# Kernel optimization log

Measured on AMD Instinct MI355X. Metric: run time of the kernel, lower is better.

The kernel has to match this reference:

```python
import jax, jax.numpy as jnp
import numpy as np

N = 80000        # nodes
E = 1280000      # edges
NG = 8           # graphs (segment ids)
F_IN = 3
NC = 20
BN_EPS = 1e-3    # keras BatchNormalization default epsilon


def setup_inputs() -> dict:
    key = jax.random.key(0)
    ks = jax.random.split(key, 16)
    inp = {}
    inp['x'] = jax.random.normal(ks[0], (N, F_IN), dtype=jnp.float32)
    inp['edge_w'] = jax.random.uniform(ks[1], (E,), dtype=jnp.float32)
    inp['src'] = jax.random.randint(ks[2], (E,), 0, N, dtype=jnp.int32)
    inp['dst'] = jax.random.randint(ks[3], (E,), 0, N, dtype=jnp.int32)
    inp['ids'] = jnp.sort(jax.random.randint(ks[4], (N,), 0, NG, dtype=jnp.int32))
    def w(k, fi, fo):
        return jax.random.normal(k, (fi, fo), dtype=jnp.float32) * (1.0 / np.sqrt(fi))
    inp['W1'] = w(ks[5], F_IN, 32); inp['b1'] = jnp.zeros((32,), jnp.float32)
    inp['W2'] = w(ks[6], 32, 32);   inp['b2'] = jnp.zeros((32,), jnp.float32)
    inp['g1'] = jnp.ones((32,), jnp.float32); inp['be1'] = jnp.zeros((32,), jnp.float32)
    inp['m1'] = jax.random.normal(ks[7], (32,), dtype=jnp.float32) * 0.1
    inp['v1'] = jax.random.uniform(ks[8], (32,), dtype=jnp.float32) + 0.5
    inp['W3'] = w(ks[9], 32, 64);   inp['b3'] = jnp.zeros((64,), jnp.float32)
    inp['W4'] = w(ks[10], 64, 64);  inp['b4'] = jnp.zeros((64,), jnp.float32)
    inp['g2'] = jnp.ones((64,), jnp.float32); inp['be2'] = jnp.zeros((64,), jnp.float32)
    inp['m2'] = jax.random.normal(ks[11], (64,), dtype=jnp.float32) * 0.1
    inp['v2'] = jax.random.uniform(ks[12], (64,), dtype=jnp.float32) + 0.5
    inp['W5'] = w(ks[13], 64, NC);  inp['b5'] = jnp.zeros((NC,), jnp.float32)
    return inp


def _gcn(x, W, b, src, dst, ew):
    # Spektral GCNConv: A_norm @ (X W) + b, with A given as edge list (src->dst).
    h = x @ W                                      # [N, Fo] dense transform first (cheaper)
    msg = h[src] * ew[:, None]                     # gather + scale  [E, Fo]
    agg = jax.ops.segment_sum(msg, dst, num_segments=N)  # scatter-add [N, Fo]
    return agg + b


def _bn(x, g, be, m, v):
    # inference-mode BatchNormalization
    return (x - m) * (g * jax.lax.rsqrt(v + BN_EPS)) + be


def _pool(x, ids):
    # per-graph global max pooling, broadcast back to nodes
    mx = jax.ops.segment_max(x, ids, num_segments=NG)   # [NG, F]
    return mx[ids]                                       # [N, F]


def reference(x, edge_w, src, dst, ids,
              W1, b1, W2, b2, g1, be1, m1, v1,
              W3, b3, W4, b4, g2, be2, m2, v2,
              W5, b5):
    h = jax.nn.relu(_gcn(x, W1, b1, src, dst, edge_w))
    h = jax.nn.relu(_gcn(h, W2, b2, src, dst, edge_w))
    h = _bn(h, g1, be1, m1, v1)
    h = _pool(h, ids)
    h = jax.nn.relu(_gcn(h, W3, b3, src, dst, edge_w))
    h = jax.nn.relu(_gcn(h, W4, b4, src, dst, edge_w))
    h = _bn(h, g2, be2, m2, v2)
    h = _pool(h, ids)
    # dropout is identity in inference
    out = jax.nn.softmax(_gcn(h, W5, b5, src, dst, edge_w), axis=-1)
    return out
```

## Files before the change

kernel.cpp:

```cpp
#include <hip/hip_runtime.h>

#define NN 80000
#define NE 1280000
#define NGR 8
#define BN_EPS 1e-3f
#define NBF 625
#define GB 1280
#define CHK 1000

typedef unsigned short ushort;
typedef __attribute__((ext_vector_type(8))) short bf16x8;
typedef __attribute__((ext_vector_type(4))) float f32x4;

__device__ __forceinline__ unsigned enc_f(float f) {
    unsigned b = __float_as_uint(f);
    return (f >= 0.f) ? (b | 0x80000000u) : ~b;
}
__device__ __forceinline__ float dec_f(unsigned u) {
    return (u & 0x80000000u) ? __uint_as_float(u & 0x7FFFFFFFu) : __uint_as_float(~u);
}
__device__ __forceinline__ ushort f2bf(float f) {
    unsigned u = __float_as_uint(f);
    unsigned r = u + 0x7FFFu + ((u >> 16) & 1u);
    return (ushort)(r >> 16);
}
__device__ __forceinline__ void fma8(float* acc, const ushort* p, float w) {
    uint4 q = *(const uint4*)p;
    acc[0] += w * __uint_as_float((q.x & 0xFFFFu) << 16);
    acc[1] += w * __uint_as_float(q.x & 0xFFFF0000u);
    acc[2] += w * __uint_as_float((q.y & 0xFFFFu) << 16);
    acc[3] += w * __uint_as_float(q.y & 0xFFFF0000u);
    acc[4] += w * __uint_as_float((q.z & 0xFFFFu) << 16);
    acc[5] += w * __uint_as_float(q.z & 0xFFFF0000u);
    acc[6] += w * __uint_as_float((q.w & 0xFFFFu) << 16);
    acc[7] += w * __uint_as_float(q.w & 0xFFFF0000u);
}

__global__ __launch_bounds__(256) void k_bhist(const int* __restrict__ dst,
                                               int* __restrict__ hcnt) {
    __shared__ int lh[NBF];
    for (int i = threadIdx.x; i < NBF; i += 256) lh[i] = 0;
    __syncthreads();
    int e0 = blockIdx.x * CHK;
    for (int e = e0 + threadIdx.x; e < e0 + CHK; e += 256)
        atomicAdd(&lh[dst[e] >> 7], 1);
    __syncthreads();
    int* row = hcnt + (size_t)blockIdx.x * NBF;
    for (int i = threadIdx.x; i < NBF; i += 256) row[i] = lh[i];
}

__global__ __launch_bounds__(256) void k_bbase1(int* __restrict__ hcnt,
                                                int* __restrict__ tot) {
    __shared__ int sm[256];
    int bin = blockIdx.x, t = threadIdx.x;
    int v[5];
    int s = 0;
    #pragma unroll
    for (int j = 0; j < 5; ++j) {
        v[j] = hcnt[(size_t)(t * 5 + j) * NBF + bin];
        s += v[j];
    }
    sm[t] = s;
    __syncthreads();
    #pragma unroll
    for (int off = 1; off < 256; off <<= 1) {
        int u = (t >= off) ? sm[t - off] : 0;
        __syncthreads();
        sm[t] += u;
        __syncthreads();
    }
    int run = sm[t] - s;
    if (t == 255) tot[bin] = sm[255];
    #pragma unroll
    for (int j = 0; j < 5; ++j) {
        hcnt[(size_t)(t * 5 + j) * NBF + bin] = run;
        run += v[j];
    }
}

__global__ __launch_bounds__(1024) void k_bbase2w(const int* __restrict__ tot,
                                                  int* __restrict__ bo,
                                                  const float* __restrict__ W2,
                                                  const float* __restrict__ W4,
                                                  ushort* __restrict__ W2t,
                                                  ushort* __restrict__ W4t) {
    __shared__ int sm[1024];
    int t = threadIdx.x;
    int v = (t < NBF) ? tot[t] : 0;
    sm[t] = v;
    __syncthreads();
    #pragma unroll
    for (int off = 1; off < 1024; off <<= 1) {
        int u = (t >= off) ? sm[t - off] : 0;
        __syncthreads();
        sm[t] += u;
        __syncthreads();
    }
    if (t < NBF) bo[t] = sm[t] - v;
    if (t == 0) bo[NBF] = NE;
    {
        int f = t >> 5, k = t & 31;
        W2t[t] = f2bf(W2[k * 32 + f]);
    }
    #pragma unroll
    for (int j = 0; j < 4; ++j) {
        int i = t + j * 1024;
        int f = i >> 6, k = i & 63;
        W4t[i] = f2bf(W4[k * 64 + f]);
    }
}

__global__ __launch_bounds__(256) void k_bfill(const int* __restrict__ src,
                                               const int* __restrict__ dst,
                                               const float* __restrict__ ew,
                                               const int* __restrict__ ids,
                                               const int* __restrict__ hcnt,
                                               const int* __restrict__ bo,
                                               int2* __restrict__ cB) {
    __shared__ int lcur[NBF];
    const int* row = hcnt + (size_t)blockIdx.x * NBF;
    for (int i = threadIdx.x; i < NBF; i += 256) lcur[i] = row[i] + bo[i];
    __syncthreads();
    int e0 = blockIdx.x * CHK;
    for (int e = e0 + threadIdx.x; e < e0 + CHK; e += 256) {
        int d = dst[e];
        int s = src[e];
        int pos = atomicAdd(&lcur[d >> 7], 1);
        cB[pos] = make_int2(s | (ids[s] << 17) | ((d & 127) << 20),
                            __float_as_int(ew[e]));
    }
}

__global__ __launch_bounds__(512) void k_insort(const int* __restrict__ bo,
                                                const int2* __restrict__ cB,
                                                const float* __restrict__ x,
                                                int* __restrict__ rp,
                                                int2* __restrict__ cE,
                                                float* __restrict__ S,
                                                float* __restrict__ AX) {
    __shared__ int lc[128];
    __shared__ int loff[128];
    __shared__ int sm[512];
    int bin = blockIdx.x, t = threadIdx.x;
    int s0 = bo[bin], s1 = bo[bin + 1];
    if (t < 128) lc[t] = 0;
    __syncthreads();
    for (int i = s0 + t; i < s1; i += 512)
        atomicAdd(&lc[(cB[i].x >> 20) & 127], 1);
    __syncthreads();
    int v = (t < 128) ? lc[t] : 0;
    sm[t] = v;
    __syncthreads();
    #pragma unroll
    for (int off = 1; off < 128; off <<= 1) {
        int u = (t >= off && t < 128) ? sm[t - off] : 0;
        __syncthreads();
        if (t < 128) sm[t] += u;
        __syncthreads();
    }
    if (t < 128) {
        loff[t] = sm[t] - v;
        rp[bin * 128 + t] = s0 + loff[t];
        lc[t] = 0;
    }
    if (bin == NBF - 1 && t == 0) rp[NN] = NE;
    __syncthreads();
    for (int i = s0 + t; i < s1; i += 512) {
        int2 a = cB[i];
        int dlow = (a.x >> 20) & 127;
        int pos = s0 + loff[dlow] + atomicAdd(&lc[dlow], 1);
        cE[pos] = make_int2((a.x & 0x1FFFF) | (((a.x >> 17) & 7) << 24), a.y);
    }
    __syncthreads();
    int n = t >> 2, q = t & 3;
    int ne0 = s0 + loff[n];
    int ne1 = ne0 + lc[n];
    float sv[8] = {0, 0, 0, 0, 0, 0, 0, 0};
    float ax0 = 0.f, ax1 = 0.f, ax2 = 0.f;
    for (int i = ne0 + q; i < ne1; i += 4) {
        int2 a = cE[i];
        float w = __int_as_float(a.y);
        int s = a.x & 0xFFFFFF;
        int gg = a.x >> 24;
        #pragma unroll
        for (int g = 0; g < 8; ++g) sv[g] += (gg == g) ? w : 0.f;
        const float* xp = x + s * 3;
        ax0 += w * xp[0]; ax1 += w * xp[1]; ax2 += w * xp[2];
    }
    #pragma unroll
    for (int g = 0; g < 8; ++g) {
        sv[g] += __shfl_xor(sv[g], 1);
        sv[g] += __shfl_xor(sv[g], 2);
    }
    ax0 += __shfl_xor(ax0, 1); ax0 += __shfl_xor(ax0, 2);
    ax1 += __shfl_xor(ax1, 1); ax1 += __shfl_xor(ax1, 2);
    ax2 += __shfl_xor(ax2, 1); ax2 += __shfl_xor(ax2, 2);
    if (q == 0) {
        int node = bin * 128 + n;
        float4* Sp = (float4*)(S + (size_t)node * 8);
        Sp[0] = make_float4(sv[0], sv[1], sv[2], sv[3]);
        Sp[1] = make_float4(sv[4], sv[5], sv[6], sv[7]);
        *(float4*)(AX + (size_t)node * 4) = make_float4(ax0, ax1, ax2, 0.f);
    }
}

__global__ __launch_bounds__(256) void k_gpl2(const float* __restrict__ AX,
                                              const float* __restrict__ W1,
                                              const float* __restrict__ b1,
                                              const ushort* __restrict__ W2t,
                                              const int* __restrict__ rp,
                                              const int2* __restrict__ cE,
                                              const int* __restrict__ ids,
                                              const float* __restrict__ b2,
                                              const float* __restrict__ g1,
                                              const float* __restrict__ be1,
                                              const float* __restrict__ m1,
                                              const float* __restrict__ v1,
                                              unsigned* __restrict__ mxe) {
    __shared__ unsigned lmx[NGR * 32];
    __shared__ ushort aggS[64 * 40];
    __shared__ int gids[64];
    int t = threadIdx.x;
    int nb = blockIdx.x * 64;
    lmx[t] = 0u;
    if (t < 64) gids[t] = ids[nb + t];
    int c = t & 3;
    float w1r0[8], w1r1[8], w1r2[8], b1c[8];
    #pragma unroll
    for (int j = 0; j < 8; ++j) {
        int f = c * 8 + j;
        w1r0[j] = W1[f]; w1r1[j] = W1[32 + f]; w1r2[j] = W1[64 + f];
        b1c[j] = b1[f];
    }
    int nl = t >> 2;
    int n = nb + nl;
    int e0 = rp[n], e1 = rp[n + 1];
    float acc[8] = {0, 0, 0, 0, 0, 0, 0, 0};
    for (int i = e0; i < e1; ++i) {
        int2 a = cE[i];
        float w = __int_as_float(a.y);
        float axv = AX[(size_t)(a.x & 0xFFFFFF) * 4 + c];
        float a0 = __shfl(axv, 0, 4);
        float a1 = __shfl(axv, 1, 4);
        float a2 = __shfl(axv, 2, 4);
        #pragma unroll
        for (int j = 0; j < 8; ++j) {
            float pre = b1c[j] + a0 * w1r0[j] + a1 * w1r1[j] + a2 * w1r2[j];
            acc[j] += w * fmaxf(pre, 0.f);
        }
    }
    #pragma unroll
    for (int j = 0; j < 8; ++j) aggS[nl * 40 + c * 8 + j] = f2bf(acc[j]);
    __syncthreads();
    int lane = t & 63, wave = t >> 6;
    int quad = lane >> 4, col = lane & 15;
    bf16x8 afr = *(const bf16x8*)(aggS + (wave * 16 + col) * 40 + quad * 8);
    #pragma unroll
    for (int nt = 0; nt < 2; ++nt) {
        bf16x8 bfr = *(const bf16x8*)(W2t + (nt * 16 + col) * 32 + quad * 8);
        f32x4 d = {0.f, 0.f, 0.f, 0.f};
        d = __builtin_amdgcn_mfma_f32_16x16x32_bf16(afr, bfr, d, 0, 0, 0);
        int f = nt * 16 + col;
        float scale = g1[f] * rsqrtf(v1[f] + BN_EPS);
        float bb = b2[f], mm = m1[f], bee = be1[f];
        #pragma unroll
        for (int r = 0; r < 4; ++r) {
            int node_l = wave * 16 + quad * 4 + r;
            float h = fmaxf(d[r] + bb, 0.f);
            float val = (h - mm) * scale + bee;
            atomicMax(&lmx[gids[node_l] * 32 + f], enc_f(val));
        }
    }
    __syncthreads();
    {
        unsigned u = lmx[t];
        if (u) atomicMax(&mxe[t], u);
    }
}

__global__ __launch_bounds__(256) void k_l34m(const float* __restrict__ S,
                                              const unsigned* __restrict__ mxe,
                                              const float* __restrict__ W3,
                                              const float* __restrict__ b3,
                                              const ushort* __restrict__ W4t,
                                              ushort* __restrict__ T) {
    __shared__ float smxs[256];
    __shared__ float HW3s[512];
    __shared__ ushort h3s[64 * 72];
    int t = threadIdx.x;
    int nb = blockIdx.x * 64;
    smxs[t] = mxe[t] ? dec_f(mxe[t]) : 0.f;
    __syncthreads();
    {
        #pragma unroll
        for (int j = 0; j < 2; ++j) {
            int i = t + j * 256;
            int g = i >> 6, f = i & 63;
            float acc = 0.f;
            #pragma unroll
            for (int k = 0; k < 32; ++k) acc += smxs[g * 32 + k] * W3[k * 64 + f];
            HW3s[i] = acc;
        }
    }
    __syncthreads();
    {
        int f = t & 63, rr = t >> 6;
        float hwc[8];
        #pragma unroll
        for (int g = 0; g < 8; ++g) hwc[g] = HW3s[g * 64 + f];
        float bb = b3[f];
        #pragma unroll
        for (int i = 0; i < 16; ++i) {
            int n = rr + i * 4;
            const float4* sp = (const float4*)(S + (size_t)(nb + n) * 8);
            float4 s0 = sp[0], s1 = sp[1];
            float acc = bb + s0.x * hwc[0] + s0.y * hwc[1] + s0.z * hwc[2] +
                        s0.w * hwc[3] + s1.x * hwc[4] + s1.y * hwc[5] +
                        s1.z * hwc[6] + s1.w * hwc[7];
            h3s[n * 72 + f] = f2bf(fmaxf(acc, 0.f));
        }
    }
    __syncthreads();
    int lane = t & 63, wave = t >> 6;
    int quad = lane >> 4, col = lane & 15;
    int mtile = wave;
    bf16x8 a0 = *(const bf16x8*)(h3s + (mtile * 16 + col) * 72 + quad * 8);
    bf16x8 a1 = *(const bf16x8*)(h3s + (mtile * 16 + col) * 72 + 32 + quad * 8);
    #pragma unroll
    for (int ntile = 0; ntile < 4; ++ntile) {
        bf16x8 b0 = *(const bf16x8*)(W4t + (ntile * 16 + col) * 64 + quad * 8);
        bf16x8 b1v = *(const bf16x8*)(W4t + (ntile * 16 + col) * 64 + 32 + quad * 8);
        f32x4 acc = {0.f, 0.f, 0.f, 0.f};
        acc = __builtin_amdgcn_mfma_f32_16x16x32_bf16(a0, b0, acc, 0, 0, 0);
        acc = __builtin_amdgcn_mfma_f32_16x16x32_bf16(a1, b1v, acc, 0, 0, 0);
        #pragma unroll
        for (int r = 0; r < 4; ++r) {
            int node = nb + mtile * 16 + quad * 4 + r;
            T[node * 64 + ntile * 16 + col] = f2bf(acc[r]);
        }
    }
}

template <int LOGF>
__global__ __launch_bounds__(256) void k_gpool(const ushort* __restrict__ th,
                                               const int* __restrict__ rp,
                                               const int2* __restrict__ cE,
                                               const int* __restrict__ ids,
                                               const float* __restrict__ b,
                                               const float* __restrict__ g,
                                               const float* __restrict__ be,
                                               const float* __restrict__ m,
                                               const float* __restrict__ v,
                                               unsigned* __restrict__ mxe) {
    const int F = 1 << LOGF;
    const int CPN = F >> 3;
    const int NPB = 256 / CPN;
    __shared__ unsigned lmx[NGR * F];
    for (int i = threadIdx.x; i < NGR * F; i += 256) lmx[i] = 0u;
    __syncthreads();
    int c = threadIdx.x & (CPN - 1);
    int n = blockIdx.x * NPB + (threadIdx.x >> (LOGF - 3));
    if (n < NN) {
        int e0 = rp[n], e1 = rp[n + 1];
        float a0[8] = {0, 0, 0, 0, 0, 0, 0, 0};
        float a1[8] = {0, 0, 0, 0, 0, 0, 0, 0};
        float a2[8] = {0, 0, 0, 0, 0, 0, 0, 0};
        float a3[8] = {0, 0, 0, 0, 0, 0, 0, 0};
        int i = e0;
        for (; i + 4 <= e1; i += 4) {
            int2 q0 = cE[i], q1 = cE[i + 1], q2 = cE[i + 2], q3 = cE[i + 3];
            fma8(a0, th + (((size_t)(q0.x & 0xFFFFFF)) << LOGF) + (c << 3), __int_as_float(q0.y));
            fma8(a1, th + (((size_t)(q1.x & 0xFFFFFF)) << LOGF) + (c << 3), __int_as_float(q1.y));
            fma8(a2, th + (((size_t)(q2.x & 0xFFFFFF)) << LOGF) + (c << 3), __int_as_float(q2.y));
            fma8(a3, th + (((size_t)(q3.x & 0xFFFFFF)) << LOGF) + (c << 3), __int_as_float(q3.y));
        }
        for (; i < e1; ++i) {
            int2 q0 = cE[i];
            fma8(a0, th + (((size_t)(q0.x & 0xFFFFFF)) << LOGF) + (c << 3), __int_as_float(q0.y));
        }
        int gg = ids[n];
        #pragma unroll
        for (int j = 0; j < 8; ++j) {
            int f = (c << 3) + j;
            float scale = g[f] * rsqrtf(v[f] + BN_EPS);
            float h = fmaxf((a0[j] + a1[j]) + (a2[j] + a3[j]) + b[f], 0.f);
            float val = (h - m[f]) * scale + be[f];
            atomicMax(&lmx[gg * F + f], enc_f(val));
        }
    }
    __syncthreads();
    for (int i = threadIdx.x; i < NGR * F; i += 256) {
        unsigned u = lmx[i];
        if (u) atomicMax(&mxe[i], u);
    }
}

__global__ __launch_bounds__(256) void k_out(const float* __restrict__ S,
                                             const unsigned* __restrict__ mxe,
                                             const float* __restrict__ W5,
                                             const float* __restrict__ b5,
                                             float* __restrict__ out) {
    __shared__ float smxs[512];
    __shared__ float hw[160];
    __shared__ float bb[20];
    int t = threadIdx.x;
    smxs[t] = mxe[t] ? dec_f(mxe[t]) : 0.f;
    smxs[t + 256] = mxe[t + 256] ? dec_f(mxe[t + 256]) : 0.f;
    if (t < 20) bb[t] = b5[t];
    __syncthreads();
    if (t < 160) {
        int g = t / 20, c = t % 20;
        float acc = 0.f;
        #pragma unroll
        for (int k = 0; k < 64; ++k) acc += smxs[g * 64 + k] * W5[k * 20 + c];
        hw[t] = acc;
    }
    __syncthreads();
    int n = blockIdx.x * 256 + t;
    if (n >= NN) return;
    const float4* sp = (const float4*)(S + (size_t)n * 8);
    float4 s0 = sp[0], s1 = sp[1];
    float sv[8] = {s0.x, s0.y, s0.z, s0.w, s1.x, s1.y, s1.z, s1.w};
    float pre[20];
    #pragma unroll
    for (int c = 0; c < 20; ++c) {
        float acc = bb[c];
        #pragma unroll
        for (int g = 0; g < 8; ++g) acc += sv[g] * hw[g * 20 + c];
        pre[c] = acc;
    }
    float mx = pre[0];
    #pragma unroll
    for (int c = 1; c < 20; ++c) mx = fmaxf(mx, pre[c]);
    float sum = 0.f;
    #pragma unroll
    for (int c = 0; c < 20; ++c) { pre[c] = __expf(pre[c] - mx); sum += pre[c]; }
    float inv = 1.f / sum;
    #pragma unroll
    for (int c = 0; c < 20; ++c) out[n * 20 + c] = pre[c] * inv;
}

extern "C" void kernel_launch(void* const* d_in, const int* in_sizes, int n_in,
                              void* d_out, int out_size, void* d_ws, size_t ws_size,
                              hipStream_t stream) {
    const float* x   = (const float*)d_in[0];
    const float* ew  = (const float*)d_in[1];
    const int*   src = (const int*)d_in[2];
    const int*   dst = (const int*)d_in[3];
    const int*   ids = (const int*)d_in[4];
    const float* W1 = (const float*)d_in[5];  const float* b1 = (const float*)d_in[6];
    const float* W2 = (const float*)d_in[7];  const float* b2 = (const float*)d_in[8];
    const float* g1 = (const float*)d_in[9];  const float* be1 = (const float*)d_in[10];
    const float* m1 = (const float*)d_in[11]; const float* v1 = (const float*)d_in[12];
    const float* W3 = (const float*)d_in[13]; const float* b3 = (const float*)d_in[14];
    const float* W4 = (const float*)d_in[15]; const float* b4 = (const float*)d_in[16];
    const float* g2 = (const float*)d_in[17]; const float* be2 = (const float*)d_in[18];
    const float* m2 = (const float*)d_in[19]; const float* v2 = (const float*)d_in[20];
    const float* W5 = (const float*)d_in[21]; const float* b5 = (const float*)d_in[22];
    float* out = (float*)d_out;

    char* p = (char*)d_ws;
    float*  S    = (float*)p;  p += (size_t)NN * 8 * 4;
    ushort* T    = (ushort*)p; p += (size_t)NN * 64 * 2;
    float*  AX   = (float*)p;  p += (size_t)NN * 4 * 4;
    int*    rp   = (int*)p;    p += (size_t)(NN + 16) * 4;
    int*    hcnt = (int*)p;    p += (size_t)GB * NBF * 4;
    int*    tot  = (int*)p;    p += 1024 * 4;
    int*    bo   = (int*)p;    p += 1024 * 4;
    int2*   cB   = (int2*)p;   p += (size_t)NE * 8;
    int2*   cE   = (int2*)p;   p += (size_t)NE * 8;
    unsigned* MXE1 = (unsigned*)p; p += 256 * 4;
    unsigned* MXE2 = (unsigned*)p; p += 512 * 4;
    ushort* W2t  = (ushort*)p; p += 1024 * 2;
    ushort* W4t  = (ushort*)p; p += 4096 * 2;

    const int BS = 256;
    const int gN = (NN + BS - 1) / BS;

    hipMemsetAsync(MXE1, 0, 768 * 4, stream);
    hipLaunchKernelGGL(k_bhist, dim3(GB), dim3(BS), 0, stream, dst, hcnt);
    hipLaunchKernelGGL(k_bbase1, dim3(NBF), dim3(BS), 0, stream, hcnt, tot);
    hipLaunchKernelGGL(k_bbase2w, dim3(1), dim3(1024), 0, stream, tot, bo, W2, W4, W2t, W4t);
    hipLaunchKernelGGL(k_bfill, dim3(GB), dim3(BS), 0, stream, src, dst, ew, ids, hcnt, bo, cB);
    hipLaunchKernelGGL(k_insort, dim3(NBF), dim3(512), 0, stream, bo, cB, x, rp, cE, S, AX);

    hipLaunchKernelGGL(k_gpl2, dim3(NN / 64), dim3(BS), 0, stream, AX, W1, b1, W2t,
                       rp, cE, ids, b2, g1, be1, m1, v1, MXE1);

    hipLaunchKernelGGL(k_l34m, dim3(NN / 64), dim3(BS), 0, stream, S, MXE1, W3, b3, W4t, T);
    hipLaunchKernelGGL(k_gpool<6>, dim3(NN / 32), dim3(BS), 0, stream, T, rp, cE, ids, b4, g2, be2, m2, v2, MXE2);

    hipLaunchKernelGGL(k_out, dim3(gN), dim3(BS), 0, stream, S, MXE2, W5, b5, out);
}
```

Before: 248.3 us.

## Stage bucket scatter in shared memory with larger edge chunks per block

Raises the edges handled per block from 1000 to 2500, which cuts the number of histogram rows from 1280 to 512 and shrinks the per-bin prefix pass to match. The fill kernel now recomputes its local bin histogram, scans it in shared memory, places each edge into a locally sorted staging buffer, and then writes that buffer out so that consecutive threads store to mostly consecutive global positions. The goal is better coalescing of the scattered cB writes. The cost is an extra histogram pass, a block-wide scan and more shared-memory use, along with fewer blocks in flight.

```diff
diff --git a/kernel.cpp b/kernel.cpp
--- a/kernel.cpp
+++ b/kernel.cpp
@@ -5,8 +5,8 @@
 #define NGR 8
 #define BN_EPS 1e-3f
 #define NBF 625
-#define GB 1280
-#define CHK 1000
+#define GB 512
+#define CHK 2500
 
 typedef unsigned short ushort;
 typedef __attribute__((ext_vector_type(8))) short bf16x8;
@@ -53,11 +53,11 @@
                                                 int* __restrict__ tot) {
     __shared__ int sm[256];
     int bin = blockIdx.x, t = threadIdx.x;
-    int v[5];
+    int v[2];
     int s = 0;
     #pragma unroll
-    for (int j = 0; j < 5; ++j) {
-        v[j] = hcnt[(size_t)(t * 5 + j) * NBF + bin];
+    for (int j = 0; j < 2; ++j) {
+        v[j] = hcnt[(size_t)(t * 2 + j) * NBF + bin];
         s += v[j];
     }
     sm[t] = s;
@@ -72,8 +72,8 @@
     int run = sm[t] - s;
     if (t == 255) tot[bin] = sm[255];
     #pragma unroll
-    for (int j = 0; j < 5; ++j) {
-        hcnt[(size_t)(t * 5 + j) * NBF + bin] = run;
+    for (int j = 0; j < 2; ++j) {
+        hcnt[(size_t)(t * 2 + j) * NBF + bin] = run;
         run += v[j];
     }
 }
@@ -117,18 +117,66 @@
                                                const int* __restrict__ hcnt,
                                                const int* __restrict__ bo,
                                                int2* __restrict__ cB) {
+    __shared__ int lh[NBF];
+    __shared__ int delta[NBF];
     __shared__ int lcur[NBF];
+    __shared__ int2 srt[CHK];
+    __shared__ short sbin[CHK];
+    __shared__ int sm[256];
+    int t = threadIdx.x;
+    int e0 = blockIdx.x * CHK;
     const int* row = hcnt + (size_t)blockIdx.x * NBF;
-    for (int i = threadIdx.x; i < NBF; i += 256) lcur[i] = row[i] + bo[i];
-    __syncthreads();
-    int e0 = blockIdx.x * CHK;
-    for (int e = e0 + threadIdx.x; e < e0 + CHK; e += 256) {
+    for (int i = t; i < NBF; i += 256) lh[i] = 0;
+    __syncthreads();
+    for (int e = e0 + t; e < e0 + CHK; e += 256)
+        atomicAdd(&lh[dst[e] >> 7], 1);
+    __syncthreads();
+    int c0, c1, c2;
+    {
+        int i0 = t * 3, i1 = t * 3 + 1, i2 = t * 3 + 2;
+        c0 = (i0 < NBF) ? lh[i0] : 0;
+        c1 = (i1 < NBF) ? lh[i1] : 0;
+        c2 = (i2 < NBF) ? lh[i2] : 0;
+    }
+    int ssum = c0 + c1 + c2;
+    sm[t] = ssum;
+    __syncthreads();
+    #pragma unroll
+    for (int off = 1; off < 256; off <<= 1) {
+        int u = (t >= off) ? sm[t - off] : 0;
+        __syncthreads();
+        sm[t] += u;
+        __syncthreads();
+    }
+    {
+        int run = sm[t] - ssum;
+        int i0 = t * 3;
+        #pragma unroll
+        for (int j = 0; j < 3; ++j) {
+            int idx = i0 + j;
+            int cnt = (j == 0) ? c0 : (j == 1) ? c1 : c2;
+            if (idx < NBF) {
+                lh[idx] = run;
+                delta[idx] = row[idx] + bo[idx] - run;
+                lcur[idx] = 0;
+            }
+            run += cnt;
+        }
+    }
+    __syncthreads();
+    for (int e = e0 + t; e < e0 + CHK; e += 256) {
         int d = dst[e];
         int s = src[e];
-        int pos = atomicAdd(&lcur[d >> 7], 1);
-        cB[pos] = make_int2(s | (ids[s] << 17) | ((d & 127) << 20),
-                            __float_as_int(ew[e]));
-    }
+        int bin = d >> 7;
+        int r = atomicAdd(&lcur[bin], 1);
+        int slot = lh[bin] + r;
+        srt[slot] = make_int2(s | (ids[s] << 17) | ((d & 127) << 20),
+                              __float_as_int(ew[e]));
+        sbin[slot] = (short)bin;
+    }
+    __syncthreads();
+    for (int p = t; p < CHK; p += 256)
+        cB[delta[sbin[p]] + p] = srt[p];
 }
 
 __global__ __launch_bounds__(512) void k_insort(const int* __restrict__ bo,
```

After: 241.9 us (median of 2 runs). 2.5% less time.
